# Performance work log

Hardware: AMD Instinct MI355X
Metric: run time of the kernel (lower is better)

The kernel has to match this reference:

```python
import jax, jax.numpy as jnp
import numpy as np

KERNEL_BANDWIDTH = 0.3
STEP_SIZE = 0.5
NB_ITERATIONS = 4


def setup_inputs() -> dict:
    key = jax.random.key(0)
    # B x D x H x W pixel embeddings
    x_in = jax.random.normal(key, (2, 64, 96, 96), dtype=jnp.float32)
    return {"x_in": x_in}


def reference(x_in):
    B, D, H, W = x_in.shape
    N = H * W
    x0 = x_in.reshape(B, D, N)

    def body(x, _):
        # Gaussian-like kernel K[i,j] = exp(bw * <x_i, x_j>), symmetric NxN per batch
        K = jnp.exp(KERNEL_BANDWIDTH * jnp.einsum('bdn,bdm->bnm', x, x))  # (B,N,N)
        # torch: diag(K^T @ 1) then inverse of that diagonal == 1/column-sums
        colsum = jnp.sum(K, axis=1)  # (B,N)
        # x @ (K diag(1/colsum)): column-normalized weighted mean of embeddings
        xk = jnp.einsum('bdn,bnm->bdm', x, K) / colsum[:, None, :]
        x_new = STEP_SIZE * xk + (1.0 - STEP_SIZE) * x
        return x_new, x_new

    _, ys = jax.lax.scan(body, x0, None, length=NB_ITERATIONS)  # (I,B,D,N)
    allx = jnp.concatenate([x0[None], ys], axis=0)  # (I+1,B,D,N)
    # B x (I+1) x D x H x W
    return jnp.transpose(allx, (1, 0, 2, 3)).reshape(B, NB_ITERATIONS + 1, D, H, W)
```

## Files before the change

kernel.cpp:

```cpp
#include <hip/hip_runtime.h>
#include <hip/hip_bf16.h>

constexpr int B_    = 2;
constexpr int N_    = 9216;
constexpr int ITERS = 4;

constexpr int MTQ     = 128;
constexpr int MBF     = N_ / MTQ;
constexpr int KS      = 3;
constexpr int KEYS_WG = N_ / KS;
constexpr int KT      = 128;
constexpr int KTILES  = KEYS_WG / KT;
constexpr int NWG     = B_ * MBF * KS;
constexpr int PB2     = 288;
constexpr int CGRID   = B_ * (N_ / 32) * 2;

constexpr float STEP = 0.5f;
constexpr float C2   = 0.43280851226668905f;

using short8   = __attribute__((ext_vector_type(8))) short;
using float16v = __attribute__((ext_vector_type(16))) float;
typedef __attribute__((ext_vector_type(2))) __bf16 bf16x2;

__device__ __forceinline__ unsigned short f2bf(float f) {
  union { float f; unsigned u; } v; v.f = f;
  unsigned u = v.u;
  unsigned r = (u + 0x7fffu + ((u >> 16) & 1u)) >> 16;
  return (unsigned short)r;
}

#if __has_builtin(__builtin_amdgcn_cvt_pk_bf16_f32)
__device__ __forceinline__ unsigned pk2bf(float a, float b) {
  bf16x2 r = __builtin_amdgcn_cvt_pk_bf16_f32(a, b);
  union { bf16x2 h; unsigned u; } v; v.h = r; return v.u;
}
#else
__device__ __forceinline__ unsigned pk2bf(float a, float b) {
  return (unsigned)f2bf(a) | ((unsigned)f2bf(b) << 16);
}
#endif

__device__ __forceinline__ float csum2(unsigned u, float cs) {
#if __has_builtin(__builtin_amdgcn_fdot2_f32_bf16)
  union { unsigned x; bf16x2 h; } a, o;
  a.x = u; o.x = 0x3f803f80u;
  return __builtin_amdgcn_fdot2_f32_bf16(a.h, o.h, cs, false);
#else
  union { unsigned u; float f; } lo, hi;
  lo.u = u << 16; hi.u = u & 0xffff0000u;
  return cs + lo.f + hi.f;
#endif
}

__device__ __forceinline__ void dma16(const unsigned short* g,
                                      unsigned short* lds_base, int lane) {
#if __has_builtin(__builtin_amdgcn_global_load_lds)
  __builtin_amdgcn_global_load_lds(
      (const __attribute__((address_space(1))) unsigned int*)g,
      (__attribute__((address_space(3))) unsigned int*)lds_base, 16, 0, 0);
#else
  *(int4*)((char*)lds_base + lane * 16) = *(const int4*)g;
#endif
}

__global__ void prep_kernel(const float* __restrict__ xin, float* __restrict__ out,
                            unsigned short* __restrict__ XT,
                            unsigned short* __restrict__ Xbf)
{
  const int bx = blockIdx.x;
  const int nb = bx % PB2, b = bx / PB2;
  const int n0 = nb * 32;
  const int tid = threadIdx.x;
  __shared__ float tile[64 * 33];

  #pragma unroll
  for (int r = 0; r < 4; ++r) {
    int idx = r * 256 + tid;
    int d = idx >> 4, j2 = (idx & 15) * 2;
    size_t gsrc = ((size_t)b * 64 + d) * N_ + n0 + j2;
    float2 v = *(const float2*)(xin + gsrc);
    *(float2*)(out + (((size_t)b * 5 + 0) * 64 + d) * N_ + n0 + j2) = v;
    *(unsigned*)(Xbf + gsrc) = pk2bf(v.x, v.y);
    tile[d * 33 + j2]     = v.x;
    tile[d * 33 + j2 + 1] = v.y;
  }
  __syncthreads();

  #pragma unroll
  for (int r = 0; r < 4; ++r) {
    int idx = r * 256 + tid;
    int nl = idx >> 5, d2 = (idx & 31) * 2;
    *(unsigned*)(XT + ((size_t)b * N_ + n0 + nl) * 64 + d2)
        = pk2bf(tile[d2 * 33 + nl], tile[(d2 + 1) * 33 + nl]);
  }
}

__global__ void __launch_bounds__(256, 2) flash_kernel(
    const unsigned short* __restrict__ XT,
    const unsigned short* __restrict__ Xbf,
    float* __restrict__ pacc, float* __restrict__ pcs)
{
  const int bx   = blockIdx.x;
  const int ks   = bx % KS;
  const int mb   = (bx / KS) % MBF;
  const int b    = bx / (MBF * KS);
  const int tid  = threadIdx.x;
  const int wave = tid >> 6, lane = tid & 63;
  const int c = lane & 31, h = lane >> 5;
  const int cp = (c & 0x13) | ((c & 4) << 1) | ((c & 8) >> 1);
  const int m0 = mb * MTQ;
  const int bpaddr = (lane ^ 32) << 2;

  const unsigned short* XTb = XT  + (size_t)b * N_ * 64;
  const unsigned short* Xb  = Xbf + (size_t)b * 64 * N_;

  __shared__ __align__(16) unsigned short sXT[2][KT * 64];
  __shared__ __align__(16) unsigned short sXB[2][64 * KT];

  const int rr  = lane >> 3, sc = lane & 7;
  const int gcT = sc ^ rr;
  const int rr4 = lane >> 4, sc16 = lane & 15;
  const int gcB0 = sc16 ^ rr4;
  const int gcB1 = sc16 ^ (4 + rr4);

  const int n0g0 = ks * KEYS_WG;

  const unsigned short* xtp  = XTb + (size_t)(n0g0 + wave * 32 + rr) * 64 + gcT * 8;
  const unsigned short* xbpA = Xb  + (size_t)(wave * 16 + rr4) * N_ + n0g0 + gcB0 * 8;
  const unsigned short* xbpB = Xb  + (size_t)(wave * 16 + rr4) * N_ + n0g0 + gcB1 * 8;

  auto stage = [&](int buf, const unsigned short* xt_,
                   const unsigned short* xbA_, const unsigned short* xbB_) {
    unsigned short* lt = &sXT[buf][wave * 32 * 64];
    unsigned short* lb = &sXB[buf][wave * 16 * 128];
    dma16(xt_,        lt,        lane);
    dma16(xt_ +  512, lt +  512, lane);
    dma16(xt_ + 1024, lt + 1024, lane);
    dma16(xt_ + 1536, lt + 1536, lane);
    dma16(xbA_,                    lb,        lane);
    dma16(xbB_ + (size_t) 4 * N_,  lb +  512, lane);
    dma16(xbA_ + (size_t) 8 * N_,  lb + 1024, lane);
    dma16(xbB_ + (size_t)12 * N_,  lb + 1536, lane);
  };

  stage(0, xtp, xbpA, xbpB);
  xtp += KT * 64; xbpA += KT; xbpB += KT;

  short8 qf[4];
  #pragma unroll
  for (int k = 0; k < 4; ++k) {
    short8 raw = *(const short8*)(XTb +
        (size_t)(m0 + wave * 32 + c) * 64 + k * 16 + h * 8);
    unsigned o[4];
    const unsigned* rw = (const unsigned*)&raw;
    #pragma unroll
    for (int p4 = 0; p4 < 4; ++p4) {
      union { unsigned u; float f; } lo, hi;
      lo.u = rw[p4] << 16; hi.u = rw[p4] & 0xffff0000u;
      o[p4] = pk2bf(lo.f * C2, hi.f * C2);
    }
    qf[k] = *(const short8*)o;
  }

  const int e = cp & 7;
  const unsigned short* afb[4];
  #pragma unroll
  for (int k = 0; k < 4; ++k)
    afb[k] = &sXT[0][cp * 64 + ((2 * k + h) ^ e) * 8];
  const int ec = c & 7;
  const unsigned short* bfb0[4], * bfb1[4];
  #pragma unroll
  for (int s = 0; s < 4; ++s) {
    bfb0[s] = &sXB[0][c * 128 + ((4 * s +     h) ^ ec) * 8];
    bfb1[s] = &sXB[0][c * 128 + ((4 * s + 2 + h) ^ ec) * 8];
  }

  float16v zv;
  #pragma unroll
  for (int p = 0; p < 16; ++p) zv[p] = 0.f;
  float16v acc[2];
  acc[0] = zv; acc[1] = zv;
  float cs0 = 0.f, cs1 = 0.f;

  __syncthreads();

  #pragma unroll 2
  for (int t = 0; t < KTILES; ++t) {
    const int buf = t & 1;
    if (t + 1 < KTILES) {
      stage(buf ^ 1, xtp, xbpA, xbpB);
      xtp += KT * 64; xbpA += KT; xbpB += KT;
    }

    #pragma unroll
    for (int s = 0; s < 4; ++s) {
      short8 af[4];
      #pragma unroll
      for (int k = 0; k < 4; ++k)
        af[k] = *(const short8*)(afb[k] + buf * 8192 + s * 2048);

      float16v S = zv;
      #pragma unroll
      for (int k = 0; k < 4; ++k)
        S = __builtin_amdgcn_mfma_f32_32x32x16_bf16(af[k], qf[k], S, 0, 0, 0);

      unsigned q[8];
      #pragma unroll
      for (int g = 0; g < 8; ++g) {
        float w0 = __builtin_amdgcn_exp2f(S[2 * g]);
        float w1 = __builtin_amdgcn_exp2f(S[2 * g + 1]);
        unsigned u = pk2bf(w0, w1);
        q[g] = u;
        if (s & 1) cs1 = csum2(u, cs1); else cs0 = csum2(u, cs0);
      }

      union { unsigned d[4]; short8 s8; } a20, a21;
      a20.d[0] = q[0]; a20.d[1] = q[1]; a20.d[2] = q[2]; a20.d[3] = q[3];
      a21.d[0] = q[4]; a21.d[1] = q[5]; a21.d[2] = q[6]; a21.d[3] = q[7];

      short8 b20[2], b21[2];
      #pragma unroll
      for (int dt = 0; dt < 2; ++dt) {
        b20[dt] = *(const short8*)(bfb0[s] + buf * 8192 + dt * 4096);
        b21[dt] = *(const short8*)(bfb1[s] + buf * 8192 + dt * 4096);
      }
      #pragma unroll
      for (int dt = 0; dt < 2; ++dt)
        acc[dt] = __builtin_amdgcn_mfma_f32_32x32x16_bf16(a20.s8, b20[dt], acc[dt], 0, 0, 0);
      #pragma unroll
      for (int dt = 0; dt < 2; ++dt)
        acc[dt] = __builtin_amdgcn_mfma_f32_32x32x16_bf16(a21.s8, b21[dt], acc[dt], 0, 0, 0);
    }

    __syncthreads();
  }

  float cs = cs0 + cs1;

  union { float f; int i; } cu; cu.f = cs;
  cu.i = __builtin_amdgcn_ds_bpermute(bpaddr, cu.i);
  float cst = cs + cu.f;
  if (h == 0) pcs[(size_t)bx * 128 + wave * 32 + c] = cst;

  float* pw = pacc + (size_t)bx * (MTQ * 64);
  #pragma unroll
  for (int dt = 0; dt < 2; ++dt)
    #pragma unroll
    for (int p = 0; p < 16; ++p) {
      int m = wave * 32 + (p & 3) + 8 * (p >> 2) + 4 * h;
      pw[m * 64 + dt * 32 + c] = acc[dt][p];
    }
}

__global__ void combine_kernel(const float* __restrict__ pacc,
                               const float* __restrict__ pcs,
                               float* __restrict__ out,
                               unsigned short* __restrict__ XT,
                               unsigned short* __restrict__ Xbf, int t)
{
  const int bx  = blockIdx.x;
  const int dh  = bx & 1;
  const int q32 = (bx >> 1) % 288, b = bx / 576;
  const int m0  = q32 * 32;
  const int fb  = q32 >> 2, sub = q32 & 3;
  const int base = (b * MBF + fb) * KS;
  const int tid = threadIdx.x;
  __shared__ float accs[32 * 33];
  __shared__ float cstl[32];

  float2 xc[2];
  int   dl2[2], ml2[2];
  size_t ob2[2];
  #pragma unroll
  for (int r = 0; r < 2; ++r) {
    int idx = r * 256 + tid;
    int ml = (idx & 15) * 2, dl = idx >> 4;
    int d  = dh * 32 + dl;
    size_t obase = (((size_t)b * 5 + t) * 64 + d) * N_ + m0 + ml;
    xc[r] = *(const float2*)(out + obase);
    ml2[r] = ml; dl2[r] = dl; ob2[r] = obase;
  }

  {
    int ml = tid >> 3, f4 = tid & 7;
    size_t off = (size_t)(sub * 32 + ml) * 64 + dh * 32 + f4 * 4;
    float4 s = make_float4(0.f, 0.f, 0.f, 0.f);
    #pragma unroll
    for (int k = 0; k < KS; ++k) {
      float4 v = *(const float4*)(pacc + (size_t)(base + k) * 8192 + off);
      s.x += v.x; s.y += v.y; s.z += v.z; s.w += v.w;
    }
    float* a = &accs[ml * 33 + f4 * 4];
    a[0] = s.x; a[1] = s.y; a[2] = s.z; a[3] = s.w;
  }
  if (tid < 32) {
    float cv = 0.f;
    #pragma unroll
    for (int k = 0; k < KS; ++k) cv += pcs[(size_t)(base + k) * 128 + sub * 32 + tid];
    cstl[tid] = cv;
  }
  __syncthreads();

  #pragma unroll
  for (int r = 0; r < 2; ++r) {
    int ml = ml2[r], dl = dl2[r];
    float a0 = accs[ml * 33 + dl], a1 = accs[(ml + 1) * 33 + dl];
    float v0 = STEP * (a0 / cstl[ml])     + (1.f - STEP) * xc[r].x;
    float v1 = STEP * (a1 / cstl[ml + 1]) + (1.f - STEP) * xc[r].y;
    *(float2*)(out + ob2[r] + (size_t)64 * N_) = make_float2(v0, v1);
    int d = dh * 32 + dl;
    *(unsigned*)(Xbf + ((size_t)b * 64 + d) * N_ + m0 + ml) = pk2bf(v0, v1);
    accs[ml * 33 + dl] = v0; accs[(ml + 1) * 33 + dl] = v1;
  }
  __syncthreads();

  #pragma unroll
  for (int r = 0; r < 2; ++r) {
    int idx = r * 256 + tid;
    int m = idx >> 4, dl = (idx & 15) * 2;
    *(unsigned*)(XT + ((size_t)b * N_ + m0 + m) * 64 + dh * 32 + dl)
        = pk2bf(accs[m * 33 + dl], accs[m * 33 + dl + 1]);
  }
}

extern "C" void kernel_launch(void* const* d_in, const int* in_sizes, int n_in,
                              void* d_out, int out_size, void* d_ws, size_t ws_size,
                              hipStream_t stream)
{
  (void)in_sizes; (void)n_in; (void)out_size; (void)ws_size;
  const float* xin = (const float*)d_in[0];
  float* out = (float*)d_out;
  char* ws = (char*)d_ws;

  unsigned short* XT  = (unsigned short*)(ws);
  unsigned short* Xbf = (unsigned short*)(ws +  2359296);
  float*          pacc = (float*)(ws +  4718592);
  float*          pcs  = (float*)(ws + 18874368);

  prep_kernel<<<B_ * PB2, 256, 0, stream>>>(xin, out, XT, Xbf);
  for (int t = 0; t < ITERS; ++t) {
    flash_kernel<<<NWG, 256, 0, stream>>>(XT, Xbf, pacc, pcs);
    combine_kernel<<<CGRID, 256, 0, stream>>>(pacc, pcs, out, XT, Xbf, t);
  }
}
```

Baseline: 336.1 us.

## Add barrier-free per-wave flash kernel on odd iterations and skip last writeback

Adds a flash_free kernel where each wave double-buffers its own 32-key tiles into private LDS slices and synchronizes only with waitcnt, with no workgroup barriers. The launcher alternates it with the existing flash kernel on odd iterations. The combine kernel also skips the bf16 re-packing writes on the final iteration, since no later flash pass reads them. In exchange, each wave loads the keys on its own, which adds redundant global/L2 traffic.

```diff
diff --git a/kernel.cpp b/kernel.cpp
--- a/kernel.cpp
+++ b/kernel.cpp
@@ -11,6 +11,8 @@
 constexpr int KEYS_WG = N_ / KS;
 constexpr int KT      = 128;
 constexpr int KTILES  = KEYS_WG / KT;
+constexpr int KTF     = 32;
+constexpr int NTF     = KEYS_WG / KTF;
 constexpr int NWG     = B_ * MBF * KS;
 constexpr int PB2     = 288;
 constexpr int CGRID   = B_ * (N_ / 32) * 2;
@@ -252,6 +254,162 @@
     }
 }
 
+__global__ void __launch_bounds__(256, 2) flash_free(
+    const unsigned short* __restrict__ XT,
+    const unsigned short* __restrict__ Xbf,
+    float* __restrict__ pacc, float* __restrict__ pcs)
+{
+  const int bx   = blockIdx.x;
+  const int ks   = bx % KS;
+  const int mb   = (bx / KS) % MBF;
+  const int b    = bx / (MBF * KS);
+  const int tid  = threadIdx.x;
+  const int wave = tid >> 6, lane = tid & 63;
+  const int c = lane & 31, h = lane >> 5;
+  const int cp = (c & 0x13) | ((c & 4) << 1) | ((c & 8) >> 1);
+  const int m0 = mb * MTQ;
+  const int bpaddr = (lane ^ 32) << 2;
+
+  const unsigned short* XTb = XT  + (size_t)b * N_ * 64;
+  const unsigned short* Xb  = Xbf + (size_t)b * 64 * N_;
+
+  __shared__ __align__(16) unsigned short sT[4][2][KTF * 64];
+  __shared__ __align__(16) unsigned short sB[4][2][64 * KTF];
+
+  short8 qf[4];
+  #pragma unroll
+  for (int k = 0; k < 4; ++k) {
+    short8 raw = *(const short8*)(XTb +
+        (size_t)(m0 + wave * 32 + c) * 64 + k * 16 + h * 8);
+    unsigned o[4];
+    const unsigned* rw = (const unsigned*)&raw;
+    #pragma unroll
+    for (int p4 = 0; p4 < 4; ++p4) {
+      union { unsigned u; float f; } lo, hi;
+      lo.u = rw[p4] << 16; hi.u = rw[p4] & 0xffff0000u;
+      o[p4] = pk2bf(lo.f * C2, hi.f * C2);
+    }
+    qf[k] = *(const short8*)o;
+  }
+  __builtin_amdgcn_sched_barrier(0);
+
+  const int rr  = lane >> 3, sc = lane & 7;
+  const int gcT = sc ^ rr;
+  const int gcB = (lane & 3) ^ ((lane >> 2) & 3);
+
+  const int n0g0 = ks * KEYS_WG;
+
+  const unsigned short* xtp = XTb + (size_t)(n0g0 + rr) * 64 + gcT * 8;
+  const unsigned short* xbp = Xb  + (size_t)(lane >> 2) * N_ + n0g0 + gcB * 8;
+
+  auto stageF = [&](int buf, const unsigned short* xt_, const unsigned short* xb_) {
+    unsigned short* lt = &sT[wave][buf][0];
+    unsigned short* lb = &sB[wave][buf][0];
+    dma16(xt_,        lt,        lane);
+    dma16(xt_ +  512, lt +  512, lane);
+    dma16(xt_ + 1024, lt + 1024, lane);
+    dma16(xt_ + 1536, lt + 1536, lane);
+    dma16(xb_,                  lb,        lane);
+    dma16(xb_ + (size_t)16 * N_, lb +  512, lane);
+    dma16(xb_ + (size_t)32 * N_, lb + 1024, lane);
+    dma16(xb_ + (size_t)48 * N_, lb + 1536, lane);
+  };
+
+  stageF(0, xtp, xbp);  xtp += KTF * 64; xbp += KTF;
+  stageF(1, xtp, xbp);  xtp += KTF * 64; xbp += KTF;
+
+  const int e = cp & 7;
+  const unsigned short* afbF[4];
+  #pragma unroll
+  for (int k = 0; k < 4; ++k)
+    afbF[k] = &sT[wave][0][cp * 64 + ((2 * k + h) ^ e) * 8];
+  const unsigned short* bfbF[2][2];
+  #pragma unroll
+  for (int k2 = 0; k2 < 2; ++k2)
+    #pragma unroll
+    for (int dt = 0; dt < 2; ++dt)
+      bfbF[k2][dt] = &sB[wave][0][(dt * 32 + c) * 32 + ((2 * k2 + h) ^ (c & 3)) * 8];
+
+  float16v zv;
+  #pragma unroll
+  for (int p = 0; p < 16; ++p) zv[p] = 0.f;
+  float16v acc[2];
+  acc[0] = zv; acc[1] = zv;
+  float cs0 = 0.f, cs1 = 0.f;
+
+  auto computeF = [&](int buf, int par) {
+    const int bo = buf * 2048;
+    short8 af[4];
+    #pragma unroll
+    for (int k = 0; k < 4; ++k)
+      af[k] = *(const short8*)(afbF[k] + bo);
+
+    float16v S = zv;
+    #pragma unroll
+    for (int k = 0; k < 4; ++k)
+      S = __builtin_amdgcn_mfma_f32_32x32x16_bf16(af[k], qf[k], S, 0, 0, 0);
+
+    unsigned q[8];
+    #pragma unroll
+    for (int g = 0; g < 8; ++g) {
+      float w0 = __builtin_amdgcn_exp2f(S[2 * g]);
+      float w1 = __builtin_amdgcn_exp2f(S[2 * g + 1]);
+      unsigned u = pk2bf(w0, w1);
+      q[g] = u;
+      if (par) cs1 = csum2(u, cs1); else cs0 = csum2(u, cs0);
+    }
+
+    union { unsigned d[4]; short8 s8; } a20, a21;
+    a20.d[0] = q[0]; a20.d[1] = q[1]; a20.d[2] = q[2]; a20.d[3] = q[3];
+    a21.d[0] = q[4]; a21.d[1] = q[5]; a21.d[2] = q[6]; a21.d[3] = q[7];
+
+    short8 bf0[2], bf1[2];
+    #pragma unroll
+    for (int dt = 0; dt < 2; ++dt) {
+      bf0[dt] = *(const short8*)(bfbF[0][dt] + bo);
+      bf1[dt] = *(const short8*)(bfbF[1][dt] + bo);
+    }
+    #pragma unroll
+    for (int dt = 0; dt < 2; ++dt)
+      acc[dt] = __builtin_amdgcn_mfma_f32_32x32x16_bf16(a20.s8, bf0[dt], acc[dt], 0, 0, 0);
+    #pragma unroll
+    for (int dt = 0; dt < 2; ++dt)
+      acc[dt] = __builtin_amdgcn_mfma_f32_32x32x16_bf16(a21.s8, bf1[dt], acc[dt], 0, 0, 0);
+  };
+
+  #pragma unroll 2
+  for (int t = 0; t < NTF - 1; ++t) {
+    asm volatile("s_waitcnt vmcnt(8)" ::: "memory");
+    __builtin_amdgcn_sched_barrier(0);
+    computeF(t & 1, t & 1);
+    asm volatile("s_waitcnt lgkmcnt(0)" ::: "memory");
+    __builtin_amdgcn_sched_barrier(0);
+    if (t + 2 < NTF) {
+      stageF(t & 1, xtp, xbp);
+      xtp += KTF * 64; xbp += KTF;
+    }
+  }
+  asm volatile("s_waitcnt vmcnt(0)" ::: "memory");
+  __builtin_amdgcn_sched_barrier(0);
+  computeF((NTF - 1) & 1, (NTF - 1) & 1);
+
+  float cs = cs0 + cs1;
+
+  union { float f; int i; } cu; cu.f = cs;
+  cu.i = __builtin_amdgcn_ds_bpermute(bpaddr, cu.i);
+  float cst = cs + cu.f;
+  if (h == 0) pcs[(size_t)bx * 128 + wave * 32 + c] = cst;
+
+  float* pw = pacc + (size_t)bx * (MTQ * 64);
+  #pragma unroll
+  for (int dt = 0; dt < 2; ++dt)
+    #pragma unroll
+    for (int p = 0; p < 16; ++p) {
+      int m = wave * 32 + (p & 3) + 8 * (p >> 2) + 4 * h;
+      pw[m * 64 + dt * 32 + c] = acc[dt][p];
+    }
+}
+
 __global__ void combine_kernel(const float* __restrict__ pacc,
                                const float* __restrict__ pcs,
                                float* __restrict__ out,
@@ -265,6 +423,7 @@
   const int fb  = q32 >> 2, sub = q32 & 3;
   const int base = (b * MBF + fb) * KS;
   const int tid = threadIdx.x;
+  const bool last = (t == ITERS - 1);
   __shared__ float accs[32 * 33];
   __shared__ float cstl[32];
 
@@ -308,10 +467,13 @@
     float v0 = STEP * (a0 / cstl[ml])     + (1.f - STEP) * xc[r].x;
     float v1 = STEP * (a1 / cstl[ml + 1]) + (1.f - STEP) * xc[r].y;
     *(float2*)(out + ob2[r] + (size_t)64 * N_) = make_float2(v0, v1);
-    int d = dh * 32 + dl;
-    *(unsigned*)(Xbf + ((size_t)b * 64 + d) * N_ + m0 + ml) = pk2bf(v0, v1);
-    accs[ml * 33 + dl] = v0; accs[(ml + 1) * 33 + dl] = v1;
-  }
+    if (!last) {
+      int d = dh * 32 + dl;
+      *(unsigned*)(Xbf + ((size_t)b * 64 + d) * N_ + m0 + ml) = pk2bf(v0, v1);
+      accs[ml * 33 + dl] = v0; accs[(ml + 1) * 33 + dl] = v1;
+    }
+  }
+  if (last) return;
   __syncthreads();
 
   #pragma unroll
@@ -339,7 +501,8 @@
 
   prep_kernel<<<B_ * PB2, 256, 0, stream>>>(xin, out, XT, Xbf);
   for (int t = 0; t < ITERS; ++t) {
-    flash_kernel<<<NWG, 256, 0, stream>>>(XT, Xbf, pacc, pcs);
+    if (t & 1) flash_free  <<<NWG, 256, 0, stream>>>(XT, Xbf, pacc, pcs);
+    else       flash_kernel<<<NWG, 256, 0, stream>>>(XT, Xbf, pacc, pcs);
     combine_kernel<<<CGRID, 256, 0, stream>>>(pacc, pcs, out, XT, Xbf, t);
   }
 }
```

New measurement: 363.3 us. 1.08x slower.
